# Optimization experiments

Measured on AMD Instinct MI355X. Metric: run time of the kernel, lower is better.

Reference implementation:

```python
import jax, jax.numpy as jnp
import numpy as np

ZETA = 2  # cosine-kernel power (init kwarg)
N_ATOMS = 100_000
N_FEAT = 512
N_SPECIES = 4
N_SUPPORT = 1000
N_STRUCT = 2000


def setup_inputs() -> dict:
    key = jax.random.key(0)
    k1, k2, k3, k4, k5 = jax.random.split(key, 5)
    power_spectrum = jax.random.normal(k1, (N_ATOMS, N_FEAT), dtype=jnp.float32)
    support_points = jax.random.normal(k2, (N_SPECIES, N_SUPPORT, N_FEAT), dtype=jnp.float32)
    weights = jax.random.normal(k3, (N_SPECIES, N_SUPPORT), dtype=jnp.float32)
    all_species = jax.random.randint(k4, (N_ATOMS,), 0, N_SPECIES, dtype=jnp.int64 if jax.config.jax_enable_x64 else jnp.int32)
    structure_ids = jnp.sort(jax.random.randint(k5, (N_ATOMS,), 0, N_STRUCT, dtype=jnp.int64 if jax.config.jax_enable_x64 else jnp.int32))
    return {
        "power_spectrum": power_spectrum,
        "support_points": support_points,
        "weights": weights,
        "all_species": all_species,
        "structure_ids": structure_ids,
        "num_structures": N_STRUCT,
    }


def reference(power_spectrum, support_points, weights, all_species, structure_ids, num_structures):
    # CosineKernel: rows are L2-normalized, kernel = (x_n @ sp_n^T) ** zeta.
    ps_n = power_spectrum / jnp.linalg.norm(power_spectrum, axis=1, keepdims=True)
    sp_n = support_points / jnp.linalg.norm(support_points, axis=-1, keepdims=True)

    n_species = support_points.shape[0]
    e_atom = jnp.zeros((power_spectrum.shape[0],), dtype=power_spectrum.dtype)
    # Small fixed loop over species (structurally distinct support sets).
    for s in range(n_species):
        K_s = jnp.einsum("nd,md->nm", ps_n, sp_n[s]) ** ZETA  # [N, M]
        e_s = K_s @ weights[s]                                  # [N]
        e_atom = e_atom + jnp.where(all_species == s, e_s, 0.0)
    # Sum-pool per structure (replaces the per-slice .sum(dim=0) loop).
    energy = jax.ops.segment_sum(e_atom, structure_ids, num_segments=num_structures)
    return energy[:, None]  # [n_structures, 1]
```

## Files before the change

### kernel.cpp

```cpp
#include <hip/hip_runtime.h>
#include <stdint.h>


#define NFEAT 512
#define NSPEC 4
#define QAB 128

typedef __fp16 half8 __attribute__((ext_vector_type(8)));
typedef __fp16 half2t __attribute__((ext_vector_type(2)));
typedef float f32x16 __attribute__((ext_vector_type(16)));

#define AS1 __attribute__((address_space(1)))
#define AS3 __attribute__((address_space(3)))

static __device__ __forceinline__ void gload_lds16(const void* g, void* l) {
    __builtin_amdgcn_global_load_lds((const AS1 uint32_t*)g, (AS3 uint32_t*)l, 16, 0, 0);
}

union H2I { half2t h; int i; };
union H8V { half2t h2[4]; half8 h8; int4 i4; };

__launch_bounds__(256)
__global__ void k_zero(float* out, int ns, int* run) {
    int i = blockIdx.x * 256 + threadIdx.x;
    if (i < ns) out[i] = 0.0f;
    if (i < NSPEC) run[i] = 0;
}

__launch_bounds__(256)
__global__ void k_rownorm(const float* __restrict__ rowsrc, const float* __restrict__ numer,
                          float* __restrict__ dst, int rows) {
    int wv = (blockIdx.x * 256 + threadIdx.x) >> 6;
    int lane = threadIdx.x & 63;
    if (wv >= rows) return;
    const float4* r = (const float4*)(rowsrc + (size_t)wv * NFEAT);
    float4 v0 = r[lane];
    float4 v1 = r[lane + 64];
    float s = v0.x * v0.x + v0.y * v0.y + v0.z * v0.z + v0.w * v0.w
            + v1.x * v1.x + v1.y * v1.y + v1.z * v1.z + v1.w * v1.w;
#pragma unroll
    for (int m = 1; m < 64; m <<= 1) s += __shfl_xor(s, m);
    if (lane == 0) dst[wv] = numer[wv] / s;
}

__launch_bounds__(256)
__global__ void k_scatter(const int* __restrict__ species, int* __restrict__ run,
                          int* __restrict__ perm, int N) {
    __shared__ int lcnt[NSPEC];
    __shared__ int lbase[NSPEC];
    int t = threadIdx.x;
    if (t < NSPEC) lcnt[t] = 0;
    __syncthreads();
    int n = blockIdx.x * 256 + t;
    int s = 0, li = 0;
    bool valid = (n < N);
    if (valid) {
        s = species[n];
        li = atomicAdd(&lcnt[s], 1);
    }
    __syncthreads();
    if (t < NSPEC) lbase[t] = atomicAdd(&run[t], lcnt[t]);
    __syncthreads();
    if (valid) perm[(size_t)s * N + lbase[s] + li] = n;
}

#define MK 16
__launch_bounds__(256)
__global__ void k_computeM(const float* __restrict__ sp, const float* __restrict__ wn,
                           __fp16* __restrict__ Mh, __fp16* __restrict__ Ml, int Msup) {
    const int s = blockIdx.z;
    const int i0 = blockIdx.y * 64;
    const int j0 = blockIdx.x * 64;
    __shared__ __align__(16) float As[MK * 64];
    __shared__ __align__(16) float Bs[MK * 64];
    const float* A = sp + (size_t)s * Msup * NFEAT;
    const float* wv = wn + s * Msup;
    const int t = threadIdx.x;
    const int tx = t & 15, ty = t >> 4;
    float acc[4][4] = {{0.f}};
    for (int m0 = 0; m0 < Msup; m0 += MK) {
        __syncthreads();
#pragma unroll
        for (int it = 0; it < 4; ++it) {
            int kt = (t >> 6) * 4 + it;
            int c = t & 63;
            int m = m0 + kt;
            float av = 0.f, bv = 0.f;
            if (m < Msup) {
                av = A[(size_t)m * NFEAT + i0 + c];
                bv = A[(size_t)m * NFEAT + j0 + c] * wv[m];
            }
            As[kt * 64 + c] = av;
            Bs[kt * 64 + c] = bv;
        }
        __syncthreads();
#pragma unroll
        for (int kt = 0; kt < MK; ++kt) {
            float4 a = *(const float4*)&As[kt * 64 + ty * 4];
            float4 b = *(const float4*)&Bs[kt * 64 + tx * 4];
            float aa[4] = {a.x, a.y, a.z, a.w};
            float bb[4] = {b.x, b.y, b.z, b.w};
#pragma unroll
            for (int i = 0; i < 4; ++i)
#pragma unroll
                for (int j = 0; j < 4; ++j) acc[i][j] += aa[i] * bb[j];
        }
    }
    const size_t base = (size_t)s * NFEAT * NFEAT;
    char* Hq = (char*)(Mh + base);
    char* Lq = (char*)(Ml + base);
#pragma unroll
    for (int i = 0; i < 4; ++i) {
        int row = i0 + ty * 4 + i;
        int jst = j0 + tx * 4;
        float a0 = acc[i][0], a1 = acc[i][1], a2 = acc[i][2], a3 = acc[i][3];
        half2t h01 = __builtin_amdgcn_cvt_pkrtz(a0, a1);
        half2t h23 = __builtin_amdgcn_cvt_pkrtz(a2, a3);
        float r0 = (a0 - (float)h01[0]) * 2048.f;
        float r1 = (a1 - (float)h01[1]) * 2048.f;
        float r2 = (a2 - (float)h23[0]) * 2048.f;
        float r3 = (a3 - (float)h23[1]) * 2048.f;
        half2t l01 = __builtin_amdgcn_cvt_pkrtz(r0, r1);
        half2t l23 = __builtin_amdgcn_cvt_pkrtz(r2, r3);
        int slot = (jst >> 3) ^ (row & 7);
        size_t off = (size_t)row * 1024 + (size_t)(slot << 4) + (size_t)((jst & 4) * 2);
        H2I c0, c1, c2, c3;
        c0.h = h01; c1.h = h23; c2.h = l01; c3.h = l23;
        int2 hv; hv.x = c0.i; hv.y = c1.i;
        int2 lv; lv.x = c2.i; lv.y = c3.i;
        *(int2*)(Hq + off) = hv;
        *(int2*)(Lq + off) = lv;
    }
}

__launch_bounds__(256, 1)
__global__ void k_qform(const float* __restrict__ X,
                        const __fp16* __restrict__ Mh, const __fp16* __restrict__ Ml,
                        const int* __restrict__ perm, const int* __restrict__ run,
                        const int* __restrict__ sid,
                        float* __restrict__ out, int N) {
    const int s = blockIdx.z;
    const int cnt = run[s];
    const int p0 = blockIdx.x * QAB;
    if (p0 >= cnt) return;
    __shared__ __align__(16) char lds[131072];

    const int t = threadIdx.x;
    const int w = t >> 6;
    const int l = t & 63;
    const int la = l & 31;
    const int g = l >> 5;

    int p = p0 + w * 32 + la;
    bool valid = (p < cnt);
    int pc = valid ? p : (cnt - 1);
    int id = perm[(size_t)s * N + pc];
    const float* xrow = X + (size_t)id * NFEAT;

    const char* mh_base = (const char*)(Mh + (size_t)s * NFEAT * NFEAT);
    const char* ml_base = (const char*)(Ml + (size_t)s * NFEAT * NFEAT);

#define STAGE(buf, ks) { \
    const char* gh_ = mh_base + (ks) * 32768; \
    const char* gl_ = ml_base + (ks) * 32768; \
    char* lb_ = lds + (buf) * 65536; \
    _Pragma("unroll") \
    for (int i_ = 0; i_ < 8; ++i_) { \
        int off_ = w * 8192 + i_ * 1024; \
        gload_lds16(gh_ + off_ + l * 16, lb_ + off_); \
        gload_lds16(gl_ + off_ + l * 16, lb_ + 32768 + off_); \
    } }

    STAGE(0, 0)

    half8 xbh[32], xbl[32];
    float nrm = 0.f;
#pragma unroll
    for (int jh = 0; jh < 32; ++jh) {
        const float4* pA = (const float4*)(xrow + jh * 16 + g * 8);
        float4 v0 = pA[0], v1 = pA[1];
        float xv[8] = {v0.x, v0.y, v0.z, v0.w, v1.x, v1.y, v1.z, v1.w};
        H8V uh, ul;
#pragma unroll
        for (int q = 0; q < 4; ++q) {
            float a = xv[2 * q], b = xv[2 * q + 1];
            half2t hp = __builtin_amdgcn_cvt_pkrtz(a, b);
            float ra = (a - (float)hp[0]) * 2048.f;
            float rb = (b - (float)hp[1]) * 2048.f;
            half2t lp = __builtin_amdgcn_cvt_pkrtz(ra, rb);
            uh.h2[q] = hp; ul.h2[q] = lp;
            nrm += a * a + b * b;
        }
        xbh[jh] = uh.h8;
        xbl[jh] = ul.h8;
    }

    float ebuf = 0.f;
    __syncthreads();

#pragma unroll
    for (int ks = 0; ks < 16; ++ks) {
        if (ks < 15) STAGE((ks + 1) & 1, ks + 1)

        H8V u0h, u0l, u1h, u1l;
        u0h.h8 = xbh[2 * ks];     u0l.h8 = xbl[2 * ks];
        u1h.h8 = xbh[2 * ks + 1]; u1l.h8 = xbl[2 * ks + 1];
        int4 F0h = u0h.i4, F0l = u0l.i4, F1h = u1h.i4, F1l = u1l.i4;
        int s0h0 = __shfl_xor(F0h.x, 32), s0h1 = __shfl_xor(F0h.y, 32);
        int s0h2 = __shfl_xor(F0h.z, 32), s0h3 = __shfl_xor(F0h.w, 32);
        int s0l0 = __shfl_xor(F0l.x, 32), s0l1 = __shfl_xor(F0l.y, 32);
        int s0l2 = __shfl_xor(F0l.z, 32), s0l3 = __shfl_xor(F0l.w, 32);
        int s1h0 = __shfl_xor(F1h.x, 32), s1h1 = __shfl_xor(F1h.y, 32);
        int s1h2 = __shfl_xor(F1h.z, 32), s1h3 = __shfl_xor(F1h.w, 32);
        int s1l0 = __shfl_xor(F1l.x, 32), s1l1 = __shfl_xor(F1l.y, 32);
        int s1l2 = __shfl_xor(F1l.z, 32), s1l3 = __shfl_xor(F1l.w, 32);
        bool hi = (g != 0);
        int Qa0h = hi ? s0h2 : F0h.x, Qb0h = hi ? s0h3 : F0h.y;
        int Qc0h = hi ? F0h.z : s0h0, Qd0h = hi ? F0h.w : s0h1;
        int Qa0l = hi ? s0l2 : F0l.x, Qb0l = hi ? s0l3 : F0l.y;
        int Qc0l = hi ? F0l.z : s0l0, Qd0l = hi ? F0l.w : s0l1;
        int Qa1h = hi ? s1h2 : F1h.x, Qb1h = hi ? s1h3 : F1h.y;
        int Qc1h = hi ? F1h.z : s1h0, Qd1h = hi ? F1h.w : s1h1;
        int Qa1l = hi ? s1l2 : F1l.x, Qb1l = hi ? s1l3 : F1l.y;
        int Qc1l = hi ? F1l.z : s1l0, Qd1l = hi ? F1l.w : s1l1;
        float xc[16];
#define XC2(QH, QL, o0, o1) { H2I qh_, ql_; qh_.i = (QH); ql_.i = (QL); \
        xc[o0] = (float)qh_.h[0] + (float)ql_.h[0] * (1.f/2048.f); \
        xc[o1] = (float)qh_.h[1] + (float)ql_.h[1] * (1.f/2048.f); }
        XC2(Qa0h, Qa0l, 0, 1)   XC2(Qb0h, Qb0l, 2, 3)
        XC2(Qc0h, Qc0l, 4, 5)   XC2(Qd0h, Qd0l, 6, 7)
        XC2(Qa1h, Qa1l, 8, 9)   XC2(Qb1h, Qb1l, 10, 11)
        XC2(Qc1h, Qc1l, 12, 13) XC2(Qd1h, Qd1l, 14, 15)
#undef XC2

        const char* mb = lds + (ks & 1) * 65536;
        f32x16 z0 = {}, z1 = {}, z2 = {};
#pragma unroll
        for (int jh = 0; jh < 32; ++jh) {
            int slot = (2 * jh + g) ^ (la & 7);
            int boff = la * 1024 + slot * 16;
            half8 Ah = *(const half8*)(mb + boff);
            half8 Al = *(const half8*)(mb + 32768 + boff);
            z0 = __builtin_amdgcn_mfma_f32_32x32x16_f16(Ah, xbh[jh], z0, 0, 0, 0);
            z1 = __builtin_amdgcn_mfma_f32_32x32x16_f16(Ah, xbl[jh], z1, 0, 0, 0);
            z2 = __builtin_amdgcn_mfma_f32_32x32x16_f16(Al, xbh[jh], z2, 0, 0, 0);
        }
#pragma unroll
        for (int r = 0; r < 16; ++r) {
            float z = z0[r] + (z1[r] + z2[r]) * (1.f / 2048.f);
            ebuf = fmaf(xc[r], z, ebuf);
        }
        __syncthreads();
    }

    float ef = ebuf + __shfl_xor(ebuf, 32);
    float nf = nrm + __shfl_xor(nrm, 32);
    if (g == 0 && valid) {
        atomicAdd(&out[sid[id]], ef / nf);
    }
#undef STAGE
}

extern "C" void kernel_launch(void* const* d_in, const int* in_sizes, int n_in,
                              void* d_out, int out_size, void* d_ws, size_t ws_size,
                              hipStream_t stream) {
    const float* ps      = (const float*)d_in[0];
    const float* sp      = (const float*)d_in[1];
    const float* w       = (const float*)d_in[2];
    const int*   species = (const int*)d_in[3];
    const int*   sid     = (const int*)d_in[4];
    float* out = (float*)d_out;

    const int S    = NSPEC;
    const int F    = NFEAT;
    const int Msup = in_sizes[2] / S;
    const int N    = in_sizes[0] / F;
    const int NS   = out_size;

    __fp16* Mh = (__fp16*)d_ws;
    __fp16* Ml = Mh + (size_t)S * F * F;
    float* wn  = (float*)(Ml + (size_t)S * F * F);
    int* run   = (int*)(wn + (size_t)S * Msup);
    int* perm  = run + 64;

    (void)n_in; (void)ws_size;

    k_zero<<<dim3((NS + 255) / 256), dim3(256), 0, stream>>>(out, NS, run);
    k_rownorm<<<dim3((S * Msup + 3) / 4), dim3(256), 0, stream>>>(sp, w, wn, S * Msup);
    k_scatter<<<dim3((N + 255) / 256), dim3(256), 0, stream>>>(species, run, perm, N);
    k_computeM<<<dim3(F / 64, F / 64, S), dim3(256), 0, stream>>>(sp, wn, Mh, Ml, Msup);
    k_qform<<<dim3((N + QAB - 1) / QAB, 1, S), dim3(256), 0, stream>>>(
        ps, Mh, Ml, perm, run, sid, out, N);
}
```

Baseline: 647.7 us.

## Restructure quadratic-form kernel into tiled GEMM with LDS-staged atom and M tiles

The quadratic-form kernel now tiles M·x as a proper 2D GEMM. Each wave computes 64 M-rows by 64 atoms, with both the M tiles and the fp16-split atom tiles staged through a smaller double-buffered LDS. Previously each wave held all 512 features of its atoms in registers against a full 32K M slab. The smaller LDS footprint and launch bound of 2 are meant to raise occupancy and reuse each M tile across more atoms. In exchange, x is reread from global memory for the final dot product, per-atom energy and norm go through extra atomic buffers, and a finalize kernel is added.

```diff
diff --git a/kernel.cpp b/kernel.cpp
--- a/kernel.cpp
+++ b/kernel.cpp
@@ -4,7 +4,6 @@
 
 #define NFEAT 512
 #define NSPEC 4
-#define QAB 128
 
 typedef __fp16 half8 __attribute__((ext_vector_type(8)));
 typedef __fp16 half2t __attribute__((ext_vector_type(2)));
@@ -21,10 +20,11 @@
 union H8V { half2t h2[4]; half8 h8; int4 i4; };
 
 __launch_bounds__(256)
-__global__ void k_zero(float* out, int ns, int* run) {
+__global__ void k_zero(float* out, int ns, int* run, float* e_acc, float* nrm_acc, int N) {
     int i = blockIdx.x * 256 + threadIdx.x;
     if (i < ns) out[i] = 0.0f;
     if (i < NSPEC) run[i] = 0;
+    if (i < N) { e_acc[i] = 0.f; nrm_acc[i] = 0.f; }
 }
 
 __launch_bounds__(256)
@@ -67,7 +67,7 @@
 #define MK 16
 __launch_bounds__(256)
 __global__ void k_computeM(const float* __restrict__ sp, const float* __restrict__ wn,
-                           __fp16* __restrict__ Mh, __fp16* __restrict__ Ml, int Msup) {
+                           __fp16* __restrict__ Ah_g, __fp16* __restrict__ Al_g, int Msup) {
     const int s = blockIdx.z;
     const int i0 = blockIdx.y * 64;
     const int j0 = blockIdx.x * 64;
@@ -106,13 +106,12 @@
                 for (int j = 0; j < 4; ++j) acc[i][j] += aa[i] * bb[j];
         }
     }
-    const size_t base = (size_t)s * NFEAT * NFEAT;
-    char* Hq = (char*)(Mh + base);
-    char* Lq = (char*)(Ml + base);
+    char* Hq = (char*)Ah_g + (size_t)s * 524288;
+    char* Lq = (char*)Al_g + (size_t)s * 524288;
 #pragma unroll
     for (int i = 0; i < 4; ++i) {
-        int row = i0 + ty * 4 + i;
-        int jst = j0 + tx * 4;
+        int r = i0 + ty * 4 + i;
+        int c = j0 + tx * 4;
         float a0 = acc[i][0], a1 = acc[i][1], a2 = acc[i][2], a3 = acc[i][3];
         half2t h01 = __builtin_amdgcn_cvt_pkrtz(a0, a1);
         half2t h23 = __builtin_amdgcn_cvt_pkrtz(a2, a3);
@@ -122,8 +121,9 @@
         float r3 = (a3 - (float)h23[1]) * 2048.f;
         half2t l01 = __builtin_amdgcn_cvt_pkrtz(r0, r1);
         half2t l23 = __builtin_amdgcn_cvt_pkrtz(r2, r3);
-        int slot = (jst >> 3) ^ (row & 7);
-        size_t off = (size_t)row * 1024 + (size_t)(slot << 4) + (size_t)((jst & 4) * 2);
+        size_t off = (size_t)((r >> 7) * 16 + (c >> 5)) * 8192
+                   + (size_t)(((c >> 3) & 3) * 2048) + (size_t)((r & 127) * 16)
+                   + (size_t)((c & 7) * 2);
         H2I c0, c1, c2, c3;
         c0.h = h01; c1.h = h23; c2.h = l01; c3.h = l23;
         int2 hv; hv.x = c0.i; hv.y = c1.i;
@@ -133,132 +133,186 @@
     }
 }
 
-__launch_bounds__(256, 1)
+__launch_bounds__(256, 2)
 __global__ void k_qform(const float* __restrict__ X,
-                        const __fp16* __restrict__ Mh, const __fp16* __restrict__ Ml,
+                        const __fp16* __restrict__ Ah_g, const __fp16* __restrict__ Al_g,
                         const int* __restrict__ perm, const int* __restrict__ run,
-                        const int* __restrict__ sid,
-                        float* __restrict__ out, int N) {
+                        float* __restrict__ e_acc, float* __restrict__ nrm_acc, int N) {
     const int s = blockIdx.z;
     const int cnt = run[s];
-    const int p0 = blockIdx.x * QAB;
+    const int p0 = blockIdx.x * 128;
     if (p0 >= cnt) return;
-    __shared__ __align__(16) char lds[131072];
+    __shared__ __align__(16) char lds[65536];
 
     const int t = threadIdx.x;
     const int w = t >> 6;
     const int l = t & 63;
     const int la = l & 31;
-    const int g = l >> 5;
-
-    int p = p0 + w * 32 + la;
-    bool valid = (p < cnt);
-    int pc = valid ? p : (cnt - 1);
-    int id = perm[(size_t)s * N + pc];
-    const float* xrow = X + (size_t)id * NFEAT;
-
-    const char* mh_base = (const char*)(Mh + (size_t)s * NFEAT * NFEAT);
-    const char* ml_base = (const char*)(Ml + (size_t)s * NFEAT * NFEAT);
-
-#define STAGE(buf, ks) { \
-    const char* gh_ = mh_base + (ks) * 32768; \
-    const char* gl_ = ml_base + (ks) * 32768; \
-    char* lb_ = lds + (buf) * 65536; \
+    const int g  = l >> 5;
+    const int wj = w >> 1;
+    const int wa = w & 1;
+
+    int idv[2]; bool valid[2];
+#pragma unroll
+    for (int at = 0; at < 2; ++at) {
+        int p = p0 + wa * 64 + at * 32 + la;
+        valid[at] = (p < cnt);
+        idv[at] = perm[(size_t)s * N + (valid[at] ? p : (cnt - 1))];
+    }
+    const int h = t & 1;
+    {
+    }
+    int pst = p0 + (t >> 1);
+    int idst = perm[(size_t)s * N + ((pst < cnt) ? pst : (cnt - 1))];
+    const float* xst_base = X + (size_t)idst * NFEAT + h * 16;
+
+    const char* ahb = (const char*)Ah_g + (size_t)s * 524288;
+    const char* alb = (const char*)Al_g + (size_t)s * 524288;
+
+    f32x16 z0[2][2] = {{{0.f}}}, zc[2][2] = {{{0.f}}};
+    float e_l[2] = {0.f, 0.f}, n_l[2] = {0.f, 0.f};
+
+#define STAGE_A(buf, st_) { \
+    char* lb_ = lds + (buf) * 32768; \
+    const char* gh_ = ahb + (size_t)(st_) * 8192; \
+    const char* gl_ = alb + (size_t)(st_) * 8192; \
     _Pragma("unroll") \
-    for (int i_ = 0; i_ < 8; ++i_) { \
-        int off_ = w * 8192 + i_ * 1024; \
-        gload_lds16(gh_ + off_ + l * 16, lb_ + off_); \
-        gload_lds16(gl_ + off_ + l * 16, lb_ + 32768 + off_); \
+    for (int i_ = 0; i_ < 2; ++i_) { \
+        int o_ = w * 2048 + i_ * 1024 + l * 16; \
+        gload_lds16(gh_ + o_, lb_ + o_); \
+        gload_lds16(gl_ + o_, lb_ + 8192 + o_); \
     } }
 
-    STAGE(0, 0)
-
-    half8 xbh[32], xbl[32];
-    float nrm = 0.f;
-#pragma unroll
-    for (int jh = 0; jh < 32; ++jh) {
-        const float4* pA = (const float4*)(xrow + jh * 16 + g * 8);
-        float4 v0 = pA[0], v1 = pA[1];
-        float xv[8] = {v0.x, v0.y, v0.z, v0.w, v1.x, v1.y, v1.z, v1.w};
-        H8V uh, ul;
-#pragma unroll
-        for (int q = 0; q < 4; ++q) {
-            float a = xv[2 * q], b = xv[2 * q + 1];
-            half2t hp = __builtin_amdgcn_cvt_pkrtz(a, b);
-            float ra = (a - (float)hp[0]) * 2048.f;
-            float rb = (b - (float)hp[1]) * 2048.f;
-            half2t lp = __builtin_amdgcn_cvt_pkrtz(ra, rb);
-            uh.h2[q] = hp; ul.h2[q] = lp;
-            nrm += a * a + b * b;
-        }
-        xbh[jh] = uh.h8;
-        xbl[jh] = ul.h8;
-    }
-
-    float ebuf = 0.f;
+#define B_LOAD(st_, vv) { \
+    const float* xp_ = xst_base + ((st_) & 15) * 32; \
+    vv[0] = *(const float4*)(xp_);      vv[1] = *(const float4*)(xp_ + 4); \
+    vv[2] = *(const float4*)(xp_ + 8);  vv[3] = *(const float4*)(xp_ + 12); }
+
+#define B_WRITE(buf, vv) { \
+    char* lb_ = lds + (buf) * 32768; \
+    float xf_[16] = {vv[0].x, vv[0].y, vv[0].z, vv[0].w,  vv[1].x, vv[1].y, vv[1].z, vv[1].w, \
+                     vv[2].x, vv[2].y, vv[2].z, vv[2].w,  vv[3].x, vv[3].y, vv[3].z, vv[3].w}; \
+    H8V uh0_, ul0_, uh1_, ul1_; \
+    _Pragma("unroll") \
+    for (int q_ = 0; q_ < 4; ++q_) { \
+        float a_ = xf_[2 * q_], b_ = xf_[2 * q_ + 1]; \
+        half2t hp_ = __builtin_amdgcn_cvt_pkrtz(a_, b_); \
+        float ra_ = (a_ - (float)hp_[0]) * 2048.f; \
+        float rb_ = (b_ - (float)hp_[1]) * 2048.f; \
+        uh0_.h2[q_] = hp_; ul0_.h2[q_] = __builtin_amdgcn_cvt_pkrtz(ra_, rb_); \
+    } \
+    _Pragma("unroll") \
+    for (int q_ = 0; q_ < 4; ++q_) { \
+        float a_ = xf_[8 + 2 * q_], b_ = xf_[8 + 2 * q_ + 1]; \
+        half2t hp_ = __builtin_amdgcn_cvt_pkrtz(a_, b_); \
+        float ra_ = (a_ - (float)hp_[0]) * 2048.f; \
+        float rb_ = (b_ - (float)hp_[1]) * 2048.f; \
+        uh1_.h2[q_] = hp_; ul1_.h2[q_] = __builtin_amdgcn_cvt_pkrtz(ra_, rb_); \
+    } \
+    int al_ = t >> 1; \
+    *(half8*)(lb_ + 16384 + (h * 2    ) * 2048 + al_ * 16) = uh0_.h8; \
+    *(half8*)(lb_ + 16384 + (h * 2 + 1) * 2048 + al_ * 16) = uh1_.h8; \
+    *(half8*)(lb_ + 24576 + (h * 2    ) * 2048 + al_ * 16) = ul0_.h8; \
+    *(half8*)(lb_ + 24576 + (h * 2 + 1) * 2048 + al_ * 16) = ul1_.h8; }
+
+    {
+        float4 bv[4];
+        B_LOAD(0, bv)
+        STAGE_A(0, 0)
+        B_WRITE(0, bv)
+    }
     __syncthreads();
 
-#pragma unroll
-    for (int ks = 0; ks < 16; ++ks) {
-        if (ks < 15) STAGE((ks + 1) & 1, ks + 1)
-
-        H8V u0h, u0l, u1h, u1l;
-        u0h.h8 = xbh[2 * ks];     u0l.h8 = xbl[2 * ks];
-        u1h.h8 = xbh[2 * ks + 1]; u1l.h8 = xbl[2 * ks + 1];
-        int4 F0h = u0h.i4, F0l = u0l.i4, F1h = u1h.i4, F1l = u1l.i4;
-        int s0h0 = __shfl_xor(F0h.x, 32), s0h1 = __shfl_xor(F0h.y, 32);
-        int s0h2 = __shfl_xor(F0h.z, 32), s0h3 = __shfl_xor(F0h.w, 32);
-        int s0l0 = __shfl_xor(F0l.x, 32), s0l1 = __shfl_xor(F0l.y, 32);
-        int s0l2 = __shfl_xor(F0l.z, 32), s0l3 = __shfl_xor(F0l.w, 32);
-        int s1h0 = __shfl_xor(F1h.x, 32), s1h1 = __shfl_xor(F1h.y, 32);
-        int s1h2 = __shfl_xor(F1h.z, 32), s1h3 = __shfl_xor(F1h.w, 32);
-        int s1l0 = __shfl_xor(F1l.x, 32), s1l1 = __shfl_xor(F1l.y, 32);
-        int s1l2 = __shfl_xor(F1l.z, 32), s1l3 = __shfl_xor(F1l.w, 32);
-        bool hi = (g != 0);
-        int Qa0h = hi ? s0h2 : F0h.x, Qb0h = hi ? s0h3 : F0h.y;
-        int Qc0h = hi ? F0h.z : s0h0, Qd0h = hi ? F0h.w : s0h1;
-        int Qa0l = hi ? s0l2 : F0l.x, Qb0l = hi ? s0l3 : F0l.y;
-        int Qc0l = hi ? F0l.z : s0l0, Qd0l = hi ? F0l.w : s0l1;
-        int Qa1h = hi ? s1h2 : F1h.x, Qb1h = hi ? s1h3 : F1h.y;
-        int Qc1h = hi ? F1h.z : s1h0, Qd1h = hi ? F1h.w : s1h1;
-        int Qa1l = hi ? s1l2 : F1l.x, Qb1l = hi ? s1l3 : F1l.y;
-        int Qc1l = hi ? F1l.z : s1l0, Qd1l = hi ? F1l.w : s1l1;
-        float xc[16];
-#define XC2(QH, QL, o0, o1) { H2I qh_, ql_; qh_.i = (QH); ql_.i = (QL); \
-        xc[o0] = (float)qh_.h[0] + (float)ql_.h[0] * (1.f/2048.f); \
-        xc[o1] = (float)qh_.h[1] + (float)ql_.h[1] * (1.f/2048.f); }
-        XC2(Qa0h, Qa0l, 0, 1)   XC2(Qb0h, Qb0l, 2, 3)
-        XC2(Qc0h, Qc0l, 4, 5)   XC2(Qd0h, Qd0l, 6, 7)
-        XC2(Qa1h, Qa1l, 8, 9)   XC2(Qb1h, Qb1l, 10, 11)
-        XC2(Qc1h, Qc1l, 12, 13) XC2(Qd1h, Qd1l, 14, 15)
-#undef XC2
-
-        const char* mb = lds + (ks & 1) * 65536;
-        f32x16 z0 = {}, z1 = {}, z2 = {};
-#pragma unroll
-        for (int jh = 0; jh < 32; ++jh) {
-            int slot = (2 * jh + g) ^ (la & 7);
-            int boff = la * 1024 + slot * 16;
-            half8 Ah = *(const half8*)(mb + boff);
-            half8 Al = *(const half8*)(mb + 32768 + boff);
-            z0 = __builtin_amdgcn_mfma_f32_32x32x16_f16(Ah, xbh[jh], z0, 0, 0, 0);
-            z1 = __builtin_amdgcn_mfma_f32_32x32x16_f16(Ah, xbl[jh], z1, 0, 0, 0);
-            z2 = __builtin_amdgcn_mfma_f32_32x32x16_f16(Al, xbh[jh], z2, 0, 0, 0);
-        }
-#pragma unroll
-        for (int r = 0; r < 16; ++r) {
-            float z = z0[r] + (z1[r] + z2[r]) * (1.f / 2048.f);
-            ebuf = fmaf(xc[r], z, ebuf);
-        }
+    for (int st = 0; st < 64; ++st) {
+        const int cur = st & 1;
+        const int nxt = cur ^ 1;
+        float4 bnx[4];
+        if (st < 63) {
+            B_LOAD(st + 1, bnx)
+            STAGE_A(nxt, st + 1)
+        }
+
+        const char* bb = lds + cur * 32768;
+        __builtin_amdgcn_s_setprio(1);
+#pragma unroll
+        for (int ki = 0; ki < 2; ++ki) {
+            int ksl = ki * 2 + g;
+            int ao = ksl * 2048 + (wj * 64 + la) * 16;
+            int bo = 16384 + ksl * 2048 + (wa * 64 + la) * 16;
+            half8 Ah0 = *(const half8*)(bb + ao);
+            half8 Ah1 = *(const half8*)(bb + ao + 512);
+            half8 Al0 = *(const half8*)(bb + 8192 + ao);
+            half8 Al1 = *(const half8*)(bb + 8192 + ao + 512);
+            half8 Bh0 = *(const half8*)(bb + bo);
+            half8 Bh1 = *(const half8*)(bb + bo + 512);
+            half8 Bl0 = *(const half8*)(bb + 8192 + bo);
+            half8 Bl1 = *(const half8*)(bb + 8192 + bo + 512);
+            z0[0][0] = __builtin_amdgcn_mfma_f32_32x32x16_f16(Ah0, Bh0, z0[0][0], 0, 0, 0);
+            z0[0][1] = __builtin_amdgcn_mfma_f32_32x32x16_f16(Ah0, Bh1, z0[0][1], 0, 0, 0);
+            z0[1][0] = __builtin_amdgcn_mfma_f32_32x32x16_f16(Ah1, Bh0, z0[1][0], 0, 0, 0);
+            z0[1][1] = __builtin_amdgcn_mfma_f32_32x32x16_f16(Ah1, Bh1, z0[1][1], 0, 0, 0);
+            zc[0][0] = __builtin_amdgcn_mfma_f32_32x32x16_f16(Ah0, Bl0, zc[0][0], 0, 0, 0);
+            zc[0][1] = __builtin_amdgcn_mfma_f32_32x32x16_f16(Ah0, Bl1, zc[0][1], 0, 0, 0);
+            zc[1][0] = __builtin_amdgcn_mfma_f32_32x32x16_f16(Ah1, Bl0, zc[1][0], 0, 0, 0);
+            zc[1][1] = __builtin_amdgcn_mfma_f32_32x32x16_f16(Ah1, Bl1, zc[1][1], 0, 0, 0);
+            zc[0][0] = __builtin_amdgcn_mfma_f32_32x32x16_f16(Al0, Bh0, zc[0][0], 0, 0, 0);
+            zc[0][1] = __builtin_amdgcn_mfma_f32_32x32x16_f16(Al0, Bh1, zc[0][1], 0, 0, 0);
+            zc[1][0] = __builtin_amdgcn_mfma_f32_32x32x16_f16(Al1, Bh0, zc[1][0], 0, 0, 0);
+            zc[1][1] = __builtin_amdgcn_mfma_f32_32x32x16_f16(Al1, Bh1, zc[1][1], 0, 0, 0);
+        }
+        __builtin_amdgcn_s_setprio(0);
+
+        if ((st & 15) == 15) {
+            const int jb = st >> 4;
+#pragma unroll
+            for (int at = 0; at < 2; ++at) {
+                const float* xr = X + (size_t)idv[at] * NFEAT + jb * 128 + wj * 64 + 4 * g;
+#pragma unroll
+                for (int jt = 0; jt < 2; ++jt) {
+                    float4 x0 = *(const float4*)(xr + jt * 32);
+                    float4 x1 = *(const float4*)(xr + jt * 32 + 8);
+                    float4 x2 = *(const float4*)(xr + jt * 32 + 16);
+                    float4 x3 = *(const float4*)(xr + jt * 32 + 24);
+                    float xv[16] = {x0.x, x0.y, x0.z, x0.w,  x1.x, x1.y, x1.z, x1.w,
+                                    x2.x, x2.y, x2.z, x2.w,  x3.x, x3.y, x3.z, x3.w};
+                    float ee = 0.f, nn = 0.f;
+#pragma unroll
+                    for (int r = 0; r < 16; ++r) {
+                        float zz = z0[jt][at][r] + zc[jt][at][r] * (1.f / 2048.f);
+                        ee = fmaf(xv[r], zz, ee);
+                        nn = fmaf(xv[r], xv[r], nn);
+                    }
+                    e_l[at] += ee;
+                    n_l[at] += nn;
+#pragma unroll
+                    for (int r = 0; r < 16; ++r) { z0[jt][at][r] = 0.f; zc[jt][at][r] = 0.f; }
+                }
+            }
+        }
+
+        if (st < 63) B_WRITE(nxt, bnx)
         __syncthreads();
     }
 
-    float ef = ebuf + __shfl_xor(ebuf, 32);
-    float nf = nrm + __shfl_xor(nrm, 32);
-    if (g == 0 && valid) {
-        atomicAdd(&out[sid[id]], ef / nf);
-    }
-#undef STAGE
+#pragma unroll
+    for (int at = 0; at < 2; ++at) {
+        float eg = e_l[at] + __shfl_xor(e_l[at], 32);
+        float ng = n_l[at] + __shfl_xor(n_l[at], 32);
+        if (g == 0 && valid[at]) {
+            atomicAdd(&e_acc[idv[at]], eg);
+            atomicAdd(&nrm_acc[idv[at]], ng);
+        }
+    }
+#undef STAGE_A
+#undef B_LOAD
+#undef B_WRITE
+}
+
+__launch_bounds__(256)
+__global__ void k_finalize(const float* __restrict__ e_acc, const float* __restrict__ nrm_acc,
+                           const int* __restrict__ sid, float* __restrict__ out, int N) {
+    int n = blockIdx.x * 256 + threadIdx.x;
+    if (n < N) atomicAdd(&out[sid[n]], e_acc[n] / nrm_acc[n]);
 }
 
 extern "C" void kernel_launch(void* const* d_in, const int* in_sizes, int n_in,
@@ -277,18 +331,21 @@
     const int N    = in_sizes[0] / F;
     const int NS   = out_size;
 
-    __fp16* Mh = (__fp16*)d_ws;
-    __fp16* Ml = Mh + (size_t)S * F * F;
-    float* wn  = (float*)(Ml + (size_t)S * F * F);
+    __fp16* Ah = (__fp16*)d_ws;
+    __fp16* Al = Ah + (size_t)S * F * F;
+    float* wn  = (float*)(Al + (size_t)S * F * F);
     int* run   = (int*)(wn + (size_t)S * Msup);
     int* perm  = run + 64;
+    float* e_acc   = (float*)(perm + (size_t)S * N);
+    float* nrm_acc = e_acc + N;
 
     (void)n_in; (void)ws_size;
 
-    k_zero<<<dim3((NS + 255) / 256), dim3(256), 0, stream>>>(out, NS, run);
+    k_zero<<<dim3((N + 255) / 256), dim3(256), 0, stream>>>(out, NS, run, e_acc, nrm_acc, N);
     k_rownorm<<<dim3((S * Msup + 3) / 4), dim3(256), 0, stream>>>(sp, w, wn, S * Msup);
     k_scatter<<<dim3((N + 255) / 256), dim3(256), 0, stream>>>(species, run, perm, N);
-    k_computeM<<<dim3(F / 64, F / 64, S), dim3(256), 0, stream>>>(sp, wn, Mh, Ml, Msup);
-    k_qform<<<dim3((N + QAB - 1) / QAB, 1, S), dim3(256), 0, stream>>>(
-        ps, Mh, Ml, perm, run, sid, out, N);
-}
+    k_computeM<<<dim3(F / 64, F / 64, S), dim3(256), 0, stream>>>(sp, wn, Ah, Al, Msup);
+    k_qform<<<dim3((N + 127) / 128, 1, S), dim3(256), 0, stream>>>(
+        ps, Ah, Al, perm, run, e_acc, nrm_acc, N);
+    k_finalize<<<dim3((N + 255) / 256), dim3(256), 0, stream>>>(e_acc, nrm_acc, sid, out, N);
+}
```

Measured after the change: 626.9 us. 1.03x faster.
